# Kernel optimization log

Measured on AMD Instinct MI355X. Metric: run time of the kernel, lower is better.

## Reference

```python
import jax, jax.numpy as jnp
import numpy as np
from jax import lax

DN = ('NCHW', 'OIHW', 'NCHW')

def conv(x, w, stride=1):
    return lax.conv_general_dilated(x, w, (stride, stride), 'SAME', dimension_numbers=DN)

def setup_inputs() -> dict:
    key = jax.random.key(0)
    ks = jax.random.split(key, 8)
    B, Cin, H, W = 16, 3, 512, 512
    Cenc, Cdec, n_heads, n_classes = 64, 64, 5, 1
    s = lambda *shape: 0.05
    return {
        'x': jax.random.normal(ks[0], (B, Cin, H, W), jnp.float32),
        'cls_id': jax.random.randint(ks[1], (B,), 0, n_heads, jnp.int32),
        'enc_w': jax.random.normal(ks[2], (Cenc, Cin, 3, 3), jnp.float32) * 0.1,
        'enc_b': jax.random.normal(ks[3], (Cenc,), jnp.float32) * 0.1,
        'dec_w': jax.random.normal(ks[4], (Cdec, Cenc, 3, 3), jnp.float32) * 0.05,
        'dec_b': jax.random.normal(ks[5], (Cdec,), jnp.float32) * 0.1,
        'head_w': jax.random.normal(ks[6], (n_heads, n_classes, Cdec, 3, 3), jnp.float32) * 0.05,
        'head_b': jax.random.normal(ks[7], (n_heads, n_classes), jnp.float32) * 0.1,
    }

def reference(x, cls_id, enc_w, enc_b, dec_w, dec_b, head_w, head_b):
    # encoder: stride-2 conv + relu -> features  [B, Cenc, H/2, W/2]
    f = jax.nn.relu(conv(x, enc_w, 2) + enc_b[None, :, None, None])
    # decoder: 3x3 conv + relu -> decoder_output [B, Cdec, H/2, W/2]
    d = jax.nn.relu(conv(f, dec_w, 1) + dec_b[None, :, None, None])
    # routing: apply segmentation_head[cls_id[b]] to sample b.
    # (gather-by-id -> per-head conv -> backsort) == per-sample gathered-kernel conv
    wk = head_w[cls_id]  # [B, n_classes, Cdec, 3, 3]
    bk = head_b[cls_id]  # [B, n_classes]
    def one_sample(di, wi):  # di: [Cdec,Hd,Wd], wi: [n_classes,Cdec,3,3]
        return conv(di[None], wi, 1)[0]
    masks = jax.vmap(one_sample)(d, wk) + bk[:, :, None, None]
    return masks  # [B, n_classes, H/2, W/2]
```

## Files before the change

### kernel.cpp

```cpp
#include <hip/hip_runtime.h>
#include <stdint.h>

#define NIMG 16
#define HIN 512
#define WIN 512
#define HO 256
#define WO 256
#define HP 258
#define WP 258

typedef unsigned short bf16_t;
typedef unsigned int u32;
typedef short bf16x8 __attribute__((ext_vector_type(8)));
typedef float f32x4 __attribute__((ext_vector_type(4)));
typedef float f32x16 __attribute__((ext_vector_type(16)));


static __device__ __forceinline__ bf16_t f2bf(float f) {
    u32 u = __float_as_uint(f);
    u += 0x7FFFu + ((u >> 16) & 1u);
    return (bf16_t)(u >> 16);
}
static __device__ __forceinline__ float bf_lo(u32 u) { return __uint_as_float(u << 16); }
static __device__ __forceinline__ float bf_hi(u32 u) { return __uint_as_float(u & 0xFFFF0000u); }
static __device__ __forceinline__ u32 pack2(float a, float b) {
    return (u32)f2bf(a) | ((u32)f2bf(b) << 16);
}

__global__ void repack_w(const float* __restrict__ dec_w, const float* __restrict__ enc_w,
                         bf16_t* __restrict__ wB, bf16_t* __restrict__ wEB) {
    int i = blockIdx.x * 256 + threadIdx.x;
    if (i < 36864) {
        int j  = i & 7;
        int l  = (i >> 3) & 63;
        int q  = (i >> 9) & 1;
        int kc = (i >> 10) & 3;
        int r  = i >> 12;
        int co  = q * 32 + (l & 31);
        int pos = kc * 16 + ((l >> 5) & 1) * 8 + j;
        int ci  = (pos & 1) * 32 + (pos >> 1);
        wB[i] = f2bf(dec_w[(co * 64 + ci) * 9 + r]);
    } else if (i < 36864 + 2048) {
        int t = i - 36864;
        int j = t & 7;
        int l = (t >> 3) & 63;
        int n = (t >> 9) & 1;
        int s = (t >> 10) & 1;
        int co = n * 32 + (l & 31);
        int k  = s * 16 + ((l >> 5) & 1) * 8 + j;
        wEB[t] = (k < 27) ? f2bf(enc_w[co * 27 + k]) : (bf16_t)0;
    }
}

__global__ void zero_halo(bf16_t* __restrict__ buf, int nimg) {
    const int per_img = 1028 * 8;
    int i = blockIdx.x * 256 + threadIdx.x;
    if (i >= nimg * per_img) return;
    int z = i / per_img;
    int rem = i - z * per_img;
    int p = rem >> 3, q = rem & 7;
    int row, col;
    if (p < 258)      { row = 0;           col = p; }
    else if (p < 516) { row = 257;         col = p - 258; }
    else if (p < 772) { row = p - 516 + 1; col = 0; }
    else              { row = p - 772 + 1; col = 257; }
    *(uint4*)(buf + ((size_t)z * HP * WP + (size_t)row * WP + col) * 64 + q * 8) =
        make_uint4(0u, 0u, 0u, 0u);
}

__global__ __launch_bounds__(512) void encoder_mfma(
    const float* __restrict__ x, const bf16_t* __restrict__ wEB,
    const float* __restrict__ enc_b, bf16_t* __restrict__ f, int b0)
{
    __shared__ __align__(16) bf16_t xt[3][33][34];

    const int tid = threadIdx.x;
    const int w   = tid >> 6;
    const int l   = tid & 63;
    const int z   = blockIdx.z;
    const int b   = b0 + z;
    const int Y0  = blockIdx.y << 5;
    const int X0  = blockIdx.x << 5;

    const int col = l & 31;
    const float bias0 = enc_b[col];
    const float bias1 = enc_b[32 + col];

    const bf16x8* wv = (const bf16x8*)wEB;
    bf16x8 Bf[2][2];
    #pragma unroll
    for (int s = 0; s < 2; ++s) {
        Bf[s][0] = wv[((s * 2 + 0) << 6) + l];
        Bf[s][1] = wv[((s * 2 + 1) << 6) + l];
    }

    const float* xb = x + (size_t)b * 3 * HIN * WIN;
    for (int i = tid; i < 3267; i += 512) {
        int ci  = i / 1089;
        int rem = i - ci * 1089;
        int yy  = rem / 33, xx = rem - yy * 33;
        int iy = Y0 + yy, ix = X0 + xx;
        float v = (iy < HIN && ix < WIN)
                ? xb[(size_t)ci * HIN * WIN + (size_t)iy * WIN + ix] : 0.f;
        xt[ci][yy][xx] = f2bf(v);
    }
    __syncthreads();

    const int row = l & 31;
    const int py  = 2 * w + (row >> 4);
    const int px  = row & 15;
    const int kh  = (l >> 5) * 8;
    bf16x8 A[2];
    #pragma unroll
    for (int s = 0; s < 2; ++s) {
        #pragma unroll
        for (int j = 0; j < 8; ++j) {
            int k = s * 16 + kh + j;
            k = k < 27 ? k : 26;
            int ci  = (k * 29) >> 8;
            int tap = k - ci * 9;
            int dy  = (tap * 11) >> 5;
            int dx  = tap - dy * 3;
            A[s][j] = (short)xt[ci][2 * py + dy][2 * px + dx];
        }
    }

    f32x16 acc[2];
    acc[0] = (f32x16){0.f,0.f,0.f,0.f,0.f,0.f,0.f,0.f,0.f,0.f,0.f,0.f,0.f,0.f,0.f,0.f};
    acc[1] = acc[0];
    acc[0] = __builtin_amdgcn_mfma_f32_32x32x16_bf16(A[0], Bf[0][0], acc[0], 0, 0, 0);
    acc[1] = __builtin_amdgcn_mfma_f32_32x32x16_bf16(A[0], Bf[0][1], acc[1], 0, 0, 0);
    acc[0] = __builtin_amdgcn_mfma_f32_32x32x16_bf16(A[1], Bf[1][0], acc[0], 0, 0, 0);
    acc[1] = __builtin_amdgcn_mfma_f32_32x32x16_bf16(A[1], Bf[1][1], acc[1], 0, 0, 0);

    bf16_t* fz = f + (size_t)z * HP * WP * 64;
    const int by = blockIdx.y << 4, bx = blockIdx.x << 4;
    #pragma unroll
    for (int v = 0; v < 16; ++v) {
        const int grow = (v & 3) + 8 * (v >> 2) + 4 * (l >> 5);
        const int flat = w * 32 + grow;
        const int pyy = flat >> 4, pxx = flat & 15;
        float t0 = acc[0][v] + bias0;  t0 = t0 > 0.f ? t0 : 0.f;
        float t1 = acc[1][v] + bias1;  t1 = t1 > 0.f ? t1 : 0.f;
        *(u32*)(fz + ((size_t)(by + pyy + 1) * WP + (bx + pxx + 1)) * 64 + 2 * col) =
            pack2(t0, t1);
    }
}

__global__ __launch_bounds__(256, 4) void decoder_mfma(
    const bf16_t* __restrict__ f, const bf16_t* __restrict__ wB,
    const float* __restrict__ dec_b, bf16_t* __restrict__ d)
{
    __shared__ __align__(16) bf16_t tile[18 * 18 * 64];

    const int tid = threadIdx.x;
    const int w   = tid >> 6;
    const int l   = tid & 63;
    const int z   = blockIdx.z;
    const int y0  = blockIdx.y << 4, x0 = blockIdx.x << 4;

    const int col = l & 31;
    const float bias0 = dec_b[col];
    const float bias1 = dec_b[32 + col];

    const bf16_t* fbase = f + ((size_t)z * HP * WP + (size_t)y0 * WP + x0) * 64;
    for (int i = tid; i < 2592; i += 256) {
        int p   = i >> 3, qq = i & 7;
        int yy  = p / 18, xx = p - yy * 18;
        uint4 v = *(const uint4*)(fbase + ((size_t)yy * WP + xx) * 64 + qq * 8);
        int byteoff = (p * 128 + qq * 16) ^ ((p & 7) << 4);
        *(uint4*)((char*)tile + byteoff) = v;
    }

    f32x16 acc[2][2];
    #pragma unroll
    for (int mf = 0; mf < 2; ++mf) {
        acc[mf][0] = (f32x16){0.f,0.f,0.f,0.f,0.f,0.f,0.f,0.f,
                              0.f,0.f,0.f,0.f,0.f,0.f,0.f,0.f};
        acc[mf][1] = acc[mf][0];
    }

    __syncthreads();

    const bf16x8* wBv = (const bf16x8*)wB;
    const int ty_l = (l >> 4) & 1;
    const int tx_l = l & 15;
    const int kh16 = (l >> 5) << 4;

    #pragma unroll
    for (int r = 0; r < 9; ++r) {
        const int dy = r / 3, dx = r - 3 * (r / 3);
        bf16x8 Bf[4][2];
        #pragma unroll
        for (int kc = 0; kc < 4; ++kc) {
            Bf[kc][0] = wBv[(((r * 4 + kc) << 1) + 0) * 64 + l];
            Bf[kc][1] = wBv[(((r * 4 + kc) << 1) + 1) * 64 + l];
        }
        #pragma unroll
        for (int mf = 0; mf < 2; ++mf) {
            const int p   = (2 * (2 * w + mf) + ty_l + dy) * 18 + tx_l + dx;
            const int swz = (p & 7) << 4;
            const int pb  = p * 128 + kh16;
            #pragma unroll
            for (int kc = 0; kc < 4; ++kc) {
                bf16x8 a = *(const bf16x8*)((const char*)tile + ((pb + kc * 32) ^ swz));
                acc[mf][0] = __builtin_amdgcn_mfma_f32_32x32x16_bf16(a, Bf[kc][0], acc[mf][0], 0, 0, 0);
                acc[mf][1] = __builtin_amdgcn_mfma_f32_32x32x16_bf16(a, Bf[kc][1], acc[mf][1], 0, 0, 0);
            }
        }
    }

    bf16_t* dz = d + (size_t)z * HP * WP * 64;
    #pragma unroll
    for (int mf = 0; mf < 2; ++mf) {
        #pragma unroll
        for (int v = 0; v < 16; ++v) {
            const int grow = (v & 3) + 8 * (v >> 2) + 4 * (l >> 5);
            const int flat = (2 * w + mf) * 32 + grow;
            const int py = flat >> 4, px = flat & 15;
            float t0 = acc[mf][0][v] + bias0;  t0 = t0 > 0.f ? t0 : 0.f;
            float t1 = acc[mf][1][v] + bias1;  t1 = t1 > 0.f ? t1 : 0.f;
            *(u32*)(dz + ((size_t)(y0 + py + 1) * WP + (x0 + px + 1)) * 64 + 2 * col) =
                pack2(t0, t1);
        }
    }
}

__global__ __launch_bounds__(256, 6) void head_kernel(
    const bf16_t* __restrict__ d, const float* __restrict__ head_w,
    const float* __restrict__ head_b, const int* __restrict__ cls_id,
    float* __restrict__ out, int b0)
{
    __shared__ __align__(16) bf16_t tile[10 * 18 * 64];
    __shared__ float hw[9][64];

    const int tid = threadIdx.x;
    const int z   = blockIdx.z;
    const int b   = b0 + z;
    const int y0  = blockIdx.y << 3;
    const int x0  = blockIdx.x << 4;
    const int cls = cls_id[b];

    for (int i = tid; i < 576; i += 256) {
        int r = i >> 6, s = i & 63;
        int ci = (s & 1) * 32 + (s >> 1);
        hw[r][s] = head_w[((size_t)cls * 64 + ci) * 9 + r];
    }
    const bf16_t* dbase = d + ((size_t)z * HP * WP + (size_t)y0 * WP + x0) * 64;
    for (int i = tid; i < 1440; i += 256) {
        int p   = i >> 3, q = i & 7;
        int yy  = p / 18, xx = p - yy * 18;
        uint4 v = *(const uint4*)(dbase + ((size_t)yy * WP + xx) * 64 + q * 8);
        int byteoff = (p * 128 + q * 16) ^ ((p & 7) << 4);
        *(uint4*)((char*)tile + byteoff) = v;
    }
    __syncthreads();

    const int half = tid & 1;
    const int px   = tid >> 1;
    const int py   = px >> 4, pxx = px & 15;
    float a0 = 0.f, a1 = 0.f, a2 = 0.f, a3 = 0.f;
    #pragma unroll 1
    for (int r = 0; r < 9; ++r) {
        const int dy = r / 3, dx = r - 3 * (r / 3);
        const int p  = (py + dy) * 18 + pxx + dx;
        const int swz = (p & 7) << 4;
        const float* wr = &hw[r][0];
        #pragma unroll
        for (int qi = 0; qi < 4; ++qi) {
            const int q = 4 * half + qi;
            uint4 v = *(const uint4*)((const char*)tile + ((p * 128 + q * 16) ^ swz));
            float4 w0 = *(const float4*)(wr + q * 8);
            float4 w1 = *(const float4*)(wr + q * 8 + 4);
            a0 = fmaf(bf_lo(v.x), w0.x, fmaf(bf_hi(v.x), w0.y, a0));
            a1 = fmaf(bf_lo(v.y), w0.z, fmaf(bf_hi(v.y), w0.w, a1));
            a2 = fmaf(bf_lo(v.z), w1.x, fmaf(bf_hi(v.z), w1.y, a2));
            a3 = fmaf(bf_lo(v.w), w1.z, fmaf(bf_hi(v.w), w1.w, a3));
        }
    }
    float tot = (a0 + a1) + (a2 + a3);
    tot += __shfl_xor(tot, 1);
    if (half == 0) {
        out[(size_t)b * (HO * WO) + (size_t)(y0 + py) * WO + (x0 + pxx)] =
            head_b[cls] + tot;
    }
}

extern "C" void kernel_launch(void* const* d_in, const int* in_sizes, int n_in,
                              void* d_out, int out_size, void* d_ws, size_t ws_size,
                              hipStream_t stream) {
    const float* x      = (const float*)d_in[0];
    const int*   cls_id = (const int*)  d_in[1];
    const float* enc_w  = (const float*)d_in[2];
    const float* enc_b  = (const float*)d_in[3];
    const float* dec_w  = (const float*)d_in[4];
    const float* dec_b  = (const float*)d_in[5];
    const float* head_w = (const float*)d_in[6];
    const float* head_b = (const float*)d_in[7];
    float* out = (float*)d_out;

    const size_t WB_RESERVE = 131072;
    const size_t PER_IMG    = (size_t)HP * WP * 64 * 2;
    char* ws = (char*)d_ws;
    bf16_t* wB  = (bf16_t*)ws;
    bf16_t* wEB = (bf16_t*)(ws + 81920);

    size_t avail = (ws_size > WB_RESERVE) ? (ws_size - WB_RESERVE) : 0;
    int C = (int)(avail / (2 * PER_IMG));
    if (C < 1) C = 1;
    if (C > NIMG) C = NIMG;

    bf16_t* fbuf = (bf16_t*)(ws + WB_RESERVE);
    bf16_t* dbuf = (bf16_t*)(ws + WB_RESERVE + (size_t)C * PER_IMG);

    repack_w<<<dim3(152), 256, 0, stream>>>(dec_w, enc_w, wB, wEB);
    {
        int nthr = C * 1028 * 8;
        int nblk = (nthr + 255) / 256;
        zero_halo<<<dim3(nblk), 256, 0, stream>>>(fbuf, C);
        zero_halo<<<dim3(nblk), 256, 0, stream>>>(dbuf, C);
    }

    int n_rounds = (NIMG + C - 1) / C;
    int per = (NIMG + n_rounds - 1) / n_rounds;
    for (int b0 = 0; b0 < NIMG; b0 += per) {
        const int n = (NIMG - b0 < per) ? (NIMG - b0) : per;
        encoder_mfma<<<dim3(16, 16, n), 512, 0, stream>>>(x, wEB, enc_b, fbuf, b0);
        decoder_mfma<<<dim3(16, 16, n), 256, 0, stream>>>(fbuf, wB, dec_b, dbuf);
        head_kernel <<<dim3(16, 32, n), 256, 0, stream>>>(dbuf, head_w, head_b, cls_id, out, b0);
    }
}
```

Baseline: 230.8 us.

## Split decoder input channels into two halves with register-staged prefetch

The decoder's shared-memory tile now holds only 32 of the 64 input channels, padded to a 72-byte pixel stride instead of the XOR swizzle. The second half of the channels is loaded from global into registers while the MFMAs run on the first half, then written to LDS after a barrier and processed. This halves LDS usage per block, which may allow more resident blocks, and overlaps part of the global load with compute. The cost is two extra barriers, 6 uint4 staging registers per thread, and a padded layout whose bank-conflict behaviour differs from the swizzle.

After: 259.4 us. 1.12x slower.

```diff
diff --git a/kernel.cpp b/kernel.cpp
--- a/kernel.cpp
+++ b/kernel.cpp
@@ -151,7 +151,7 @@
     const bf16_t* __restrict__ f, const bf16_t* __restrict__ wB,
     const float* __restrict__ dec_b, bf16_t* __restrict__ d)
 {
-    __shared__ __align__(16) bf16_t tile[18 * 18 * 64];
+    __shared__ __align__(16) bf16_t tile[324 * 36];
 
     const int tid = threadIdx.x;
     const int w   = tid >> 6;
@@ -164,12 +164,12 @@
     const float bias1 = dec_b[32 + col];
 
     const bf16_t* fbase = f + ((size_t)z * HP * WP + (size_t)y0 * WP + x0) * 64;
-    for (int i = tid; i < 2592; i += 256) {
-        int p   = i >> 3, qq = i & 7;
-        int yy  = p / 18, xx = p - yy * 18;
+
+    for (int i = tid; i < 1296; i += 256) {
+        int p = i >> 2, qq = i & 3;
+        int yy = (p * 456) >> 13, xx = p - yy * 18;
         uint4 v = *(const uint4*)(fbase + ((size_t)yy * WP + xx) * 64 + qq * 8);
-        int byteoff = (p * 128 + qq * 16) ^ ((p & 7) << 4);
-        *(uint4*)((char*)tile + byteoff) = v;
+        *(uint4*)((char*)tile + p * 72 + qq * 16) = v;
     }
 
     f32x16 acc[2][2];
@@ -182,6 +182,17 @@
 
     __syncthreads();
 
+    uint4 st[6];
+    #pragma unroll
+    for (int it = 0; it < 6; ++it) {
+        int i = tid + it * 256;
+        if (i < 1296) {
+            int p = i >> 2, qq = i & 3;
+            int yy = (p * 456) >> 13, xx = p - yy * 18;
+            st[it] = *(const uint4*)(fbase + ((size_t)yy * WP + xx) * 64 + 32 + qq * 8);
+        }
+    }
+
     const bf16x8* wBv = (const bf16x8*)wB;
     const int ty_l = (l >> 4) & 1;
     const int tx_l = l & 15;
@@ -190,22 +201,54 @@
     #pragma unroll
     for (int r = 0; r < 9; ++r) {
         const int dy = r / 3, dx = r - 3 * (r / 3);
-        bf16x8 Bf[4][2];
-        #pragma unroll
-        for (int kc = 0; kc < 4; ++kc) {
-            Bf[kc][0] = wBv[(((r * 4 + kc) << 1) + 0) * 64 + l];
-            Bf[kc][1] = wBv[(((r * 4 + kc) << 1) + 1) * 64 + l];
+        bf16x8 Bf[2][2];
+        #pragma unroll
+        for (int kcl = 0; kcl < 2; ++kcl) {
+            Bf[kcl][0] = wBv[(((r * 4 + kcl) << 1) + 0) * 64 + l];
+            Bf[kcl][1] = wBv[(((r * 4 + kcl) << 1) + 1) * 64 + l];
         }
         #pragma unroll
         for (int mf = 0; mf < 2; ++mf) {
-            const int p   = (2 * (2 * w + mf) + ty_l + dy) * 18 + tx_l + dx;
-            const int swz = (p & 7) << 4;
-            const int pb  = p * 128 + kh16;
+            const int p    = (2 * (2 * w + mf) + ty_l + dy) * 18 + tx_l + dx;
+            const int base = p * 72 + kh16;
             #pragma unroll
-            for (int kc = 0; kc < 4; ++kc) {
-                bf16x8 a = *(const bf16x8*)((const char*)tile + ((pb + kc * 32) ^ swz));
-                acc[mf][0] = __builtin_amdgcn_mfma_f32_32x32x16_bf16(a, Bf[kc][0], acc[mf][0], 0, 0, 0);
-                acc[mf][1] = __builtin_amdgcn_mfma_f32_32x32x16_bf16(a, Bf[kc][1], acc[mf][1], 0, 0, 0);
+            for (int kcl = 0; kcl < 2; ++kcl) {
+                bf16x8 a = *(const bf16x8*)((const char*)tile + base + kcl * 32);
+                acc[mf][0] = __builtin_amdgcn_mfma_f32_32x32x16_bf16(a, Bf[kcl][0], acc[mf][0], 0, 0, 0);
+                acc[mf][1] = __builtin_amdgcn_mfma_f32_32x32x16_bf16(a, Bf[kcl][1], acc[mf][1], 0, 0, 0);
+            }
+        }
+    }
+
+    __syncthreads();
+    #pragma unroll
+    for (int it = 0; it < 6; ++it) {
+        int i = tid + it * 256;
+        if (i < 1296) {
+            int p = i >> 2, qq = i & 3;
+            *(uint4*)((char*)tile + p * 72 + qq * 16) = st[it];
+        }
+    }
+    __syncthreads();
+
+    #pragma unroll
+    for (int r = 0; r < 9; ++r) {
+        const int dy = r / 3, dx = r - 3 * (r / 3);
+        bf16x8 Bf[2][2];
+        #pragma unroll
+        for (int kcl = 0; kcl < 2; ++kcl) {
+            Bf[kcl][0] = wBv[(((r * 4 + 2 + kcl) << 1) + 0) * 64 + l];
+            Bf[kcl][1] = wBv[(((r * 4 + 2 + kcl) << 1) + 1) * 64 + l];
+        }
+        #pragma unroll
+        for (int mf = 0; mf < 2; ++mf) {
+            const int p    = (2 * (2 * w + mf) + ty_l + dy) * 18 + tx_l + dx;
+            const int base = p * 72 + kh16;
+            #pragma unroll
+            for (int kcl = 0; kcl < 2; ++kcl) {
+                bf16x8 a = *(const bf16x8*)((const char*)tile + base + kcl * 32);
+                acc[mf][0] = __builtin_amdgcn_mfma_f32_32x32x16_bf16(a, Bf[kcl][0], acc[mf][0], 0, 0, 0);
+                acc[mf][1] = __builtin_amdgcn_mfma_f32_32x32x16_bf16(a, Bf[kcl][1], acc[mf][1], 0, 0, 0);
             }
         }
     }
```
